# Optimization experiments

Hardware: AMD Instinct MI355X
Metric: run time of the kernel (lower is better)

The kernel has to match this reference:

```python
import jax, jax.numpy as jnp
import numpy as np

N, C, P, M = 8, 20, 8732, 16
THRESHOLD, NEG_POS_RATIO, ALPHA = 0.5, 3, 1.0


def cxcy_to_xy(c):
    return jnp.concatenate([c[..., :2] - c[..., 2:] / 2.0, c[..., :2] + c[..., 2:] / 2.0], axis=-1)


def xy_to_cxcy(xy):
    return jnp.concatenate([(xy[..., :2] + xy[..., 2:]) / 2.0, xy[..., 2:] - xy[..., :2]], axis=-1)


def cxcy_to_gcxgcy(cxcy, priors):
    g_cxcy = (cxcy[..., :2] - priors[..., :2]) / (priors[..., 2:] / 10.0)
    g_wh = jnp.log(cxcy[..., 2:] / priors[..., 2:]) * 5.0
    return jnp.concatenate([g_cxcy, g_wh], axis=-1)


def jaccard(a, b):
    # a: (M,4), b: (P,4), boundary coords -> IoU (M,P)
    lo = jnp.maximum(a[:, None, :2], b[None, :, :2])
    hi = jnp.minimum(a[:, None, 2:], b[None, :, 2:])
    inter = jnp.prod(jnp.clip(hi - lo, 0.0), axis=-1)
    area_a = jnp.prod(a[:, 2:] - a[:, :2], axis=-1)
    area_b = jnp.prod(b[:, 2:] - b[:, :2], axis=-1)
    return inter / (area_a[:, None] + area_b[None, :] - inter)


def setup_inputs() -> dict:
    key = jax.random.key(0)
    k1, k2, k3, k4, k5, k6 = jax.random.split(key, 6)
    predicted_locs = jax.random.normal(k1, (N, C, P, 4), jnp.float32)
    predicted_scores = jax.random.normal(k2, (N, C, P, 2), jnp.float32)
    # valid ground-truth boundary boxes (x1<x2, y1<y2) in [0,1]
    ctr = jax.random.uniform(k3, (N, C, M, 2), minval=0.2, maxval=0.8)
    wh = jax.random.uniform(k4, (N, C, M, 2), minval=0.05, maxval=0.3)
    boxes = jnp.concatenate([ctr - wh / 2.0, ctr + wh / 2.0], axis=-1)
    # valid priors in cxcywh (w,h > 0 so log-encoding is finite)
    pctr = jax.random.uniform(k5, (P, 2), minval=0.05, maxval=0.95)
    pwh = jax.random.uniform(k6, (P, 2), minval=0.05, maxval=0.5)
    priors_cxcy = jnp.concatenate([pctr, pwh], axis=-1)
    labels = jnp.ones((N, C, M), jnp.int32)  # binary per-class head: object label = 1
    return {
        "predicted_locs": predicted_locs,
        "predicted_scores": predicted_scores,
        "boxes": boxes,
        "labels": labels,
        "priors_cxcy": priors_cxcy,
    }


def _forward(predicted_locs, predicted_scores, boxes, priors_cxcy, labels):
    n_classes = predicted_scores.shape[1]
    n_priors = predicted_scores.shape[2]
    priors_xy = cxcy_to_xy(priors_cxcy)

    def match(b, lab):
        # b: (M,4) boundary, lab: (M,) int
        ov = jaccard(b, priors_xy)                       # (M,P)
        obj_for_prior = jnp.argmax(ov, axis=0)           # (P,)
        ov_for_prior = jnp.max(ov, axis=0)               # (P,)
        prior_for_obj = jnp.argmax(ov, axis=1)           # (M,)
        # force each object to own its best prior
        obj_for_prior = obj_for_prior.at[prior_for_obj].set(jnp.arange(b.shape[0]))
        ov_for_prior = ov_for_prior.at[prior_for_obj].set(1.0)
        cls = jnp.where(ov_for_prior < THRESHOLD, 0, lab[obj_for_prior])  # (P,)
        tl = cxcy_to_gcxgcy(xy_to_cxcy(b[obj_for_prior]), priors_cxcy)    # (P,4)
        return tl, cls

    true_locs, true_classes = jax.vmap(jax.vmap(match))(boxes, labels)  # (N,C,P,4), (N,C,P)

    pos = true_classes != 0                      # (N,C,P)
    posf = pos.astype(predicted_locs.dtype)
    n_pos_bc = posf.sum(axis=2)                  # (N,C) positives per image per class
    n_pos_c = n_pos_bc.sum(axis=0)               # (C,)

    # localization: mean L1 over positive priors (4 coords each), per class
    l1 = jnp.abs(predicted_locs - true_locs).sum(-1) * posf   # (N,C,P)
    loc_loss_c = l1.sum(axis=(0, 2)) / jnp.maximum(n_pos_c * 4.0, 1.0)

    # per-prior binary cross entropy
    logp = jax.nn.log_softmax(predicted_scores, axis=-1)      # (N,C,P,2)
    ce = -jnp.take_along_axis(logp, true_classes[..., None], axis=-1)[..., 0]  # (N,C,P)
    conf_pos_c = (ce * posf).sum(axis=(0, 2))

    # hard negative mining: sort negatives desc per (image,class) row, keep top 3*n_pos
    ce_neg = jnp.where(pos, 0.0, ce)
    ce_neg_sorted = -jnp.sort(-ce_neg, axis=-1)               # (N,C,P) descending
    n_hard = NEG_POS_RATIO * n_pos_bc                         # (N,C)
    ranks = jnp.arange(n_priors, dtype=n_hard.dtype)
    hard_mask = ranks[None, None, :] < n_hard[..., None]
    conf_hard_c = (ce_neg_sorted * hard_mask).sum(axis=(0, 2))

    safe = jnp.maximum(n_pos_c, 1.0)
    loss_c = jnp.where(
        n_pos_c > 0,
        (conf_pos_c + conf_hard_c + ALPHA * loc_loss_c) / safe,
        0.0,
    ) / n_classes
    return loss_c.sum()


def reference(predicted_locs, predicted_scores, boxes, labels, priors_cxcy):
    return _forward(predicted_locs, predicted_scores, boxes, priors_cxcy, labels)
```

## Files before the change

kernel.cpp:

```cpp
#include <hip/hip_runtime.h>
#include <math.h>

#define NN 8
#define CC 20
#define PP 8732
#define MM 16
#define NPR 3
#define ROWS (NN * CC)
#define SPLIT 12
#define CH 728
#define ABLK 256
#define FBLK 1024
#define EPT 9

#define OFF_PART  5588480
#define OFF_CST   5834240
#define OFF_RST   5857280
#define OFF_CNT   5862400

__device__ __forceinline__ float fast_rcp(float x) { return __builtin_amdgcn_rcpf(x); }
__device__ __forceinline__ float rfl(float x) {
    return __uint_as_float(__builtin_amdgcn_readfirstlane(__float_as_uint(x)));
}

__device__ __forceinline__ float lse2(float a, float b) {
    float mx = fmaxf(a, b);
    float d  = fabsf(a - b);
    return mx + __logf(1.0f + __expf(-d));
}

__global__ __launch_bounds__(ABLK) void mbox_p1(
    const float* __restrict__ locs, const float* __restrict__ scores,
    const float* __restrict__ boxes, const int* __restrict__ labels,
    const float* __restrict__ priors,
    float* __restrict__ cef,
    unsigned long long* __restrict__ partials, float* __restrict__ cstats,
    int* __restrict__ donecnt)
{
    const int row = blockIdx.x / SPLIT;
    const int chunk = blockIdx.x - row * SPLIT;
    const int tid = threadIdx.x, lane = tid & 63, wav = tid >> 6;

    if (blockIdx.x == 0 && tid == 0) *donecnt = 0;

    __shared__ float s_bcx[MM], s_bcy[MM], s_bw[MM], s_bh[MM];
    __shared__ unsigned int s_pk[4 * MM];
    __shared__ float s_rf[4 * 3];

    float bx1[MM], by1[MM], bx2[MM], by2[MM], bar[MM];
    unsigned int labm = 0;
    {
        const float* bb = boxes + (size_t)row * MM * 4;
        const int*   lb = labels + (size_t)row * MM;
#pragma unroll
        for (int m = 0; m < MM; m++) {
            float x1 = rfl(bb[m * 4 + 0]), y1 = rfl(bb[m * 4 + 1]);
            float x2 = rfl(bb[m * 4 + 2]), y2 = rfl(bb[m * 4 + 3]);
            bx1[m] = x1; by1[m] = y1; bx2[m] = x2; by2[m] = y2;
            bar[m] = rfl((x2 - x1) * (y2 - y1));
            labm |= (lb[m] != 0 ? 1u : 0u) << m;
        }
        labm = __builtin_amdgcn_readfirstlane(labm);
    }
    if (tid < MM) {
        s_bcx[tid] = (bx1[tid] + bx2[tid]) * 0.5f;
        s_bcy[tid] = (by1[tid] + by2[tid]) * 0.5f;
        s_bw[tid]  = bx2[tid] - bx1[tid];
        s_bh[tid]  = by2[tid] - by1[tid];
    }
    __syncthreads();

    const float4* pri4 = (const float4*)priors;
    const float4* loc4 = (const float4*)(locs + (size_t)row * PP * 4);
    const float2* sc2  = (const float2*)(scores + (size_t)row * PP * 2);
    float* cefr        = cef + (size_t)row * PP;

    unsigned int bestk[MM];
#pragma unroll
    for (int m = 0; m < MM; m++) bestk[m] = 0u;
    float l_np = 0.0f, l_l1 = 0.0f, l_cp = 0.0f;
    const int p0 = chunk * CH, p1e = min(p0 + CH, PP);

    float4 pr_next; float2 sc_next;
    if (p0 + tid < p1e) { pr_next = pri4[p0 + tid]; sc_next = sc2[p0 + tid]; }
    int it = 0;
    for (int p = p0 + tid; p < p1e; p += ABLK, ++it) {
        float4 pr = pr_next;
        float2 sc = sc_next;
        if (p + ABLK < p1e) { pr_next = pri4[p + ABLK]; sc_next = sc2[p + ABLK]; }
        const unsigned int lowb = ((unsigned int)(7 - it) << 8) | (unsigned int)(255 - tid);
        float hw = pr.z * 0.5f, hh = pr.w * 0.5f;
        float px1 = pr.x - hw, py1 = pr.y - hh;
        float px2 = pr.x + hw, py2 = pr.y + hh;
        float area_b = (px2 - px1) * (py2 - py1);
        unsigned int bovk = 0u;
#pragma unroll
        for (int m = 0; m < MM; m++) {
            float dx = fminf(bx2[m], px2) - fmaxf(bx1[m], px1);
            float dy = fminf(by2[m], py2) - fmaxf(by1[m], py1);
            dx = fmaxf(dx, 0.0f); dy = fmaxf(dy, 0.0f);
            float inter = dx * dy;
            float den = (bar[m] + area_b) - inter;
            float iou = inter * fast_rcp(den);
            unsigned int ib = __float_as_uint(iou);
            bovk = max(bovk, (ib & 0xFFFFFFF0u) | (unsigned int)(15 - m));
            bestk[m] = max(bestk[m], (ib & 0xFFFFF800u) | lowb);
        }
        int bm = 15 - (int)(bovk & 15u);
        bool pos = (bovk >= 0x3F000000u) && (((labm >> bm) & 1u) != 0u);
        float lse = lse2(sc.x, sc.y);
        float ce;
        if (pos) {
            float4 pl = loc4[p];
            l_np += 1.0f;
            l_cp += lse - sc.y;
            float tx = (s_bcx[bm] - pr.x) * 10.0f / pr.z;
            float ty = (s_bcy[bm] - pr.y) * 10.0f / pr.w;
            float tw = __logf(s_bw[bm] / pr.z) * 5.0f;
            float th = __logf(s_bh[bm] / pr.w) * 5.0f;
            l_l1 += fabsf(pl.x - tx) + fabsf(pl.y - ty) + fabsf(pl.z - tw) + fabsf(pl.w - th);
            ce = 0.0f;
        } else {
            ce = fmaxf(lse - sc.x, 0.0f);
        }
        cefr[p] = ce;
    }

#pragma unroll
    for (int m = 0; m < MM; m++) {
        unsigned int key = bestk[m];
#pragma unroll
        for (int off = 32; off; off >>= 1) {
            unsigned int o = __shfl_down(key, off);
            if (o > key) key = o;
        }
        if (lane == 0) s_pk[wav * MM + m] = key;
    }
#pragma unroll
    for (int off = 32; off; off >>= 1) {
        l_np += __shfl_down(l_np, off);
        l_l1 += __shfl_down(l_l1, off);
        l_cp += __shfl_down(l_cp, off);
    }
    if (lane == 0) { s_rf[wav * 3] = l_np; s_rf[wav * 3 + 1] = l_l1; s_rf[wav * 3 + 2] = l_cp; }
    __syncthreads();
    if (tid < MM) {
        unsigned int key = s_pk[tid];
        for (int w = 1; w < 4; w++) {
            unsigned int o = s_pk[w * MM + tid];
            if (o > key) key = o;
        }
        int tw  = 255 - (int)(key & 255u);
        int itw = 7 - (int)((key >> 8) & 7u);
        int pm  = p0 + itw * ABLK + tw;
        partials[((size_t)row * MM + tid) * SPLIT + chunk] =
            ((unsigned long long)(key & 0xFFFFF800u) << 32) |
            (unsigned int)(0x7fffffff - pm);
    }
    if (tid == 0) {
        float np = 0, l1 = 0, cp = 0;
        for (int w = 0; w < 4; w++) { np += s_rf[w * 3]; l1 += s_rf[w * 3 + 1]; cp += s_rf[w * 3 + 2]; }
        float* cs = cstats + ((size_t)row * SPLIT + chunk) * 3;
        cs[0] = np; cs[1] = l1; cs[2] = cp;
    }
}

__global__ __launch_bounds__(FBLK) void mbox_sel(
    const float* __restrict__ locs, const float* __restrict__ scores,
    const float* __restrict__ boxes, const int* __restrict__ labels,
    const float* __restrict__ priors,
    const float* __restrict__ cef,
    const unsigned long long* __restrict__ partials,
    const float* __restrict__ cstats, float* __restrict__ rstats,
    int* __restrict__ donecnt, float* __restrict__ out)
{
    const int row = blockIdx.x, tid = threadIdx.x, lane = tid & 63, wav = tid >> 6;

    __shared__ unsigned int s_u32[PP];
    __shared__ float s_bx1[MM], s_by1[MM], s_bx2[MM], s_by2[MM], s_bar[MM];
    __shared__ float s_bcx[MM], s_bcy[MM], s_bw[MM], s_bh[MM];
    __shared__ int s_lab[MM], s_pfo[MM];
    __shared__ float s_sum[3];
    __shared__ unsigned int s_hist[256];
    __shared__ unsigned int s_prefix, s_Kr, s_K;
    __shared__ float s_redf[16];
    __shared__ int s_redi[16];
    __shared__ int s_flag;

    if (tid < MM) {
        const float* b = boxes + ((size_t)row * MM + tid) * 4;
        float x1 = b[0], y1 = b[1], x2 = b[2], y2 = b[3];
        s_bx1[tid] = x1; s_by1[tid] = y1; s_bx2[tid] = x2; s_by2[tid] = y2;
        s_bar[tid] = (x2 - x1) * (y2 - y1);
        s_bcx[tid] = (x1 + x2) * 0.5f; s_bcy[tid] = (y1 + y2) * 0.5f;
        s_bw[tid] = x2 - x1; s_bh[tid] = y2 - y1;
        s_lab[tid] = labels[row * MM + tid];
        const unsigned long long* pr = partials + ((size_t)row * MM + tid) * SPLIT;
        unsigned long long key = pr[0];
        for (int c = 1; c < SPLIT; c++) { unsigned long long o = pr[c]; if (o > key) key = o; }
        s_pfo[tid] = 0x7fffffff - (int)(unsigned)(key & 0xffffffffull);
    }
    if (tid >= 16 && tid < 19) {
        int j = tid - 16; float s = 0;
        for (int c = 0; c < SPLIT; c++) s += cstats[((size_t)row * SPLIT + c) * 3 + j];
        s_sum[j] = s;
    }
#pragma unroll
    for (int k = 0; k < EPT; k++) {
        const int p = tid + k * FBLK;
        if (p < PP) s_u32[p] = __float_as_uint(cef[(size_t)row * PP + p]);
    }
    __syncthreads();

    const float4* pri4 = (const float4*)priors;
    const float4* loc4 = (const float4*)(locs + (size_t)row * PP * 4);
    const float2* sc2  = (const float2*)(scores + (size_t)row * PP * 2);
    float d_np = 0, d_l1 = 0, d_cp = 0;
    if (tid < MM) {
        int p = s_pfo[tid];
        bool is_last = true;
        for (int mm = tid + 1; mm < MM; mm++) if (s_pfo[mm] == p) is_last = false;
        if (is_last) {
            const float4 pr = pri4[p];
            const float4 pl = loc4[p];
            const float2 sc = sc2[p];
            float lse = lse2(sc.x, sc.y);
            float hw = pr.z * 0.5f, hh = pr.w * 0.5f;
            float px1 = pr.x - hw, py1 = pr.y - hh;
            float px2 = pr.x + hw, py2 = pr.y + hh;
            float area_b = (px2 - px1) * (py2 - py1);
            unsigned int bovk = 0u;
            for (int m = 0; m < MM; m++) {
                float dx = fminf(s_bx2[m], px2) - fmaxf(s_bx1[m], px1);
                float dy = fminf(s_by2[m], py2) - fmaxf(s_by1[m], py1);
                dx = fmaxf(dx, 0.0f); dy = fmaxf(dy, 0.0f);
                float inter = dx * dy;
                float den = (s_bar[m] + area_b) - inter;
                float iou = inter * fast_rcp(den);
                unsigned int ib = __float_as_uint(iou);
                bovk = max(bovk, (ib & 0xFFFFFFF0u) | (unsigned int)(15 - m));
            }
            int mo = 15 - (int)(bovk & 15u);
            bool waspos = (bovk >= 0x3F000000u) && (s_lab[mo] != 0);
            if (waspos) {
                d_np -= 1.0f; d_cp -= (lse - sc.y);
                float tx = (s_bcx[mo] - pr.x) * 10.0f / pr.z;
                float ty = (s_bcy[mo] - pr.y) * 10.0f / pr.w;
                float tw = __logf(s_bw[mo] / pr.z) * 5.0f;
                float th = __logf(s_bh[mo] / pr.w) * 5.0f;
                d_l1 -= fabsf(pl.x - tx) + fabsf(pl.y - ty) + fabsf(pl.z - tw) + fabsf(pl.w - th);
            }
            if (s_lab[tid] != 0) {
                d_np += 1.0f; d_cp += (lse - sc.y);
                float tx = (s_bcx[tid] - pr.x) * 10.0f / pr.z;
                float ty = (s_bcy[tid] - pr.y) * 10.0f / pr.w;
                float tw = __logf(s_bw[tid] / pr.z) * 5.0f;
                float th = __logf(s_bh[tid] / pr.w) * 5.0f;
                d_l1 += fabsf(pl.x - tx) + fabsf(pl.y - ty) + fabsf(pl.z - tw) + fabsf(pl.w - th);
                s_u32[p] = 0u;
            } else {
                s_u32[p] = __float_as_uint(fmaxf(lse - sc.x, 0.0f));
            }
        }
    }
    if (tid < 64) {
#pragma unroll
        for (int off = 32; off; off >>= 1) {
            d_np += __shfl_down(d_np, off);
            d_l1 += __shfl_down(d_l1, off);
            d_cp += __shfl_down(d_cp, off);
        }
        if (tid == 0) {
            float np = s_sum[0] + d_np;
            __hip_atomic_store(&rstats[(size_t)row * 8 + 0], np,
                               __ATOMIC_RELAXED, __HIP_MEMORY_SCOPE_AGENT);
            __hip_atomic_store(&rstats[(size_t)row * 8 + 1], s_sum[1] + d_l1,
                               __ATOMIC_RELAXED, __HIP_MEMORY_SCOPE_AGENT);
            __hip_atomic_store(&rstats[(size_t)row * 8 + 2], s_sum[2] + d_cp,
                               __ATOMIC_RELAXED, __HIP_MEMORY_SCOPE_AGENT);
            int K = NPR * (int)(np + 0.5f);
            s_K = (K > 0) ? (unsigned)K : 0u;
            s_prefix = 0u;
            s_Kr = (K > 0) ? (unsigned)K : 0u;
        }
    }
    __syncthreads();

    const unsigned int K = s_K;
    unsigned int T = 0u;
    if (K > 0u && K < PP) {
        for (int pass = 0; pass < 4; pass++) {
            const int shift = 24 - 8 * pass;
            if (tid < 256) s_hist[tid] = 0u;
            __syncthreads();
            const unsigned int pref   = s_prefix;
            const unsigned int maskhi = (pass == 0) ? 0u : (0xffffffffu << (shift + 8));
#pragma unroll
            for (int k = 0; k < EPT; k++) {
                const int p = tid + k * FBLK;
                unsigned int u = (p < PP) ? s_u32[p] : 0u;
                if ((u & maskhi) == pref) atomicAdd(&s_hist[(u >> shift) & 255u], 1u);
            }
            __syncthreads();
            if (wav == 0) {
                unsigned int Kr = s_Kr;
                unsigned int h0 = s_hist[lane * 4 + 0];
                unsigned int h1 = s_hist[lane * 4 + 1];
                unsigned int h2 = s_hist[lane * 4 + 2];
                unsigned int h3 = s_hist[lane * 4 + 3];
                unsigned int c3 = h3;
                unsigned int c2 = h3 + h2;
                unsigned int c1 = c2 + h1;
                unsigned int c0 = c1 + h0;
                unsigned int suf = c0;
#pragma unroll
                for (int off = 1; off < 64; off <<= 1) {
                    unsigned int o = __shfl_down(suf, off);
                    if (lane + off < 64) suf += o;
                }
                unsigned int above = suf - c0;
                int cand = -1;
                unsigned int G = 0;
                if      (c3 + above >= Kr) { cand = lane * 4 + 3; G = above + c3 - h3; }
                else if (c2 + above >= Kr) { cand = lane * 4 + 2; G = above + c2 - h2; }
                else if (c1 + above >= Kr) { cand = lane * 4 + 1; G = above + c1 - h1; }
                else if (c0 + above >= Kr) { cand = lane * 4 + 0; G = above + c0 - h0; }
                int best = cand;
#pragma unroll
                for (int off = 32; off; off >>= 1) best = max(best, __shfl_down(best, off));
                best = __shfl(best, 0);
                if (cand == best && cand >= 0) {
                    s_Kr = Kr - G;
                    s_prefix = pref | ((unsigned int)best << shift);
                }
            }
            __syncthreads();
        }
        T = s_prefix;
    }

    float sgt = 0.0f; int cgt = 0;
    if (K > 0u) {
#pragma unroll
        for (int k = 0; k < EPT; k++) {
            const int p = tid + k * FBLK;
            unsigned int u = (p < PP) ? s_u32[p] : 0u;
            if (u > T) { sgt += __uint_as_float(u); cgt++; }
        }
    }
#pragma unroll
    for (int off = 32; off; off >>= 1) {
        sgt += __shfl_down(sgt, off);
        cgt += __shfl_down(cgt, off);
    }
    if (lane == 0) { s_redf[wav] = sgt; s_redi[wav] = cgt; }
    __syncthreads();
    if (tid == 0) {
        float s = 0; int cnt = 0;
        for (int w = 0; w < 16; w++) { s += s_redf[w]; cnt += s_redi[w]; }
        float chard = (K > 0u) ? (s + (float)(int)(K - (unsigned)cnt) * __uint_as_float(T)) : 0.0f;
        __hip_atomic_store(&rstats[(size_t)row * 8 + 4], chard,
                           __ATOMIC_RELAXED, __HIP_MEMORY_SCOPE_AGENT);
        int old = __hip_atomic_fetch_add(donecnt, 1, __ATOMIC_ACQ_REL,
                                         __HIP_MEMORY_SCOPE_AGENT);
        s_flag = (old == ROWS - 1) ? 1 : 0;
    }
    __syncthreads();
    if (!s_flag) return;

    if (tid < 64) {
        int c = tid;
        float loss = 0.0f;
        if (c < CC) {
            float np = 0, l1 = 0, cp = 0, ch = 0;
            for (int n = 0; n < NN; n++) {
                const float* s = rstats + ((size_t)(n * CC + c)) * 8;
                np += __hip_atomic_load(&s[0], __ATOMIC_ACQUIRE, __HIP_MEMORY_SCOPE_AGENT);
                l1 += __hip_atomic_load(&s[1], __ATOMIC_ACQUIRE, __HIP_MEMORY_SCOPE_AGENT);
                cp += __hip_atomic_load(&s[2], __ATOMIC_ACQUIRE, __HIP_MEMORY_SCOPE_AGENT);
                ch += __hip_atomic_load(&s[4], __ATOMIC_ACQUIRE, __HIP_MEMORY_SCOPE_AGENT);
            }
            float loc = l1 / fmaxf(np * 4.0f, 1.0f);
            float val = (np > 0.0f) ? (cp + ch + loc) / fmaxf(np, 1.0f) : 0.0f;
            loss = val / (float)CC;
        }
#pragma unroll
        for (int off = 32; off; off >>= 1) loss += __shfl_down(loss, off);
        if (tid == 0) out[0] = loss;
    }
}

extern "C" void kernel_launch(void* const* d_in, const int* in_sizes, int n_in,
                              void* d_out, int out_size, void* d_ws, size_t ws_size,
                              hipStream_t stream) {
    const float* locs   = (const float*)d_in[0];
    const float* scores = (const float*)d_in[1];
    const float* boxes  = (const float*)d_in[2];
    const int*   labels = (const int*)d_in[3];
    const float* priors = (const float*)d_in[4];
    float* out = (float*)d_out;

    char* ws = (char*)d_ws;
    float* cef                   = (float*)ws;
    unsigned long long* partials = (unsigned long long*)(ws + OFF_PART);
    float* cstats                = (float*)(ws + OFF_CST);
    float* rstats                = (float*)(ws + OFF_RST);
    int* donecnt                 = (int*)(ws + OFF_CNT);

    mbox_p1<<<ROWS * SPLIT, ABLK, 0, stream>>>(locs, scores, boxes, labels, priors,
                                               cef, partials, cstats, donecnt);
    mbox_sel<<<ROWS, FBLK, 0, stream>>>(locs, scores, boxes, labels, priors,
                                        cef, partials, cstats, rstats, donecnt, out);
}
```

Baseline: 128.7 us.

## Halve p1 split, vectorize cef load, per-wave histograms, separate finalize kernel

Reduces the matching kernel split from 12 to 6 chunks per row, so each block covers twice as many priors. The selection kernel now loads its scores into LDS with uint4 vector loads. The radix-select histogram becomes 16 per-wave copies to cut LDS atomic contention, at the cost of an extra merge step and sync per pass. The last-block done-counter with atomics is replaced by a third tiny finalize kernel, which adds a launch but removes the global atomic and fence traffic.

```diff
diff --git a/kernel.cpp b/kernel.cpp
--- a/kernel.cpp
+++ b/kernel.cpp
@@ -7,16 +7,16 @@
 #define MM 16
 #define NPR 3
 #define ROWS (NN * CC)
-#define SPLIT 12
-#define CH 728
+#define SPLIT 6
+#define CH 1456
 #define ABLK 256
 #define FBLK 1024
 #define EPT 9
+#define NV4 2183
 
 #define OFF_PART  5588480
-#define OFF_CST   5834240
-#define OFF_RST   5857280
-#define OFF_CNT   5862400
+#define OFF_CST   5711360
+#define OFF_RST   5722880
 
 __device__ __forceinline__ float fast_rcp(float x) { return __builtin_amdgcn_rcpf(x); }
 __device__ __forceinline__ float rfl(float x) {
@@ -34,14 +34,11 @@
     const float* __restrict__ boxes, const int* __restrict__ labels,
     const float* __restrict__ priors,
     float* __restrict__ cef,
-    unsigned long long* __restrict__ partials, float* __restrict__ cstats,
-    int* __restrict__ donecnt)
+    unsigned long long* __restrict__ partials, float* __restrict__ cstats)
 {
     const int row = blockIdx.x / SPLIT;
     const int chunk = blockIdx.x - row * SPLIT;
     const int tid = threadIdx.x, lane = tid & 63, wav = tid >> 6;
-
-    if (blockIdx.x == 0 && tid == 0) *donecnt = 0;
 
     __shared__ float s_bcx[MM], s_bcy[MM], s_bw[MM], s_bh[MM];
     __shared__ unsigned int s_pk[4 * MM];
@@ -171,21 +168,20 @@
     const float* __restrict__ priors,
     const float* __restrict__ cef,
     const unsigned long long* __restrict__ partials,
-    const float* __restrict__ cstats, float* __restrict__ rstats,
-    int* __restrict__ donecnt, float* __restrict__ out)
+    const float* __restrict__ cstats, float* __restrict__ rstats)
 {
     const int row = blockIdx.x, tid = threadIdx.x, lane = tid & 63, wav = tid >> 6;
 
     __shared__ unsigned int s_u32[PP];
+    __shared__ unsigned int s_hist[16][257];
+    __shared__ unsigned int s_h[256];
     __shared__ float s_bx1[MM], s_by1[MM], s_bx2[MM], s_by2[MM], s_bar[MM];
     __shared__ float s_bcx[MM], s_bcy[MM], s_bw[MM], s_bh[MM];
     __shared__ int s_lab[MM], s_pfo[MM];
     __shared__ float s_sum[3];
-    __shared__ unsigned int s_hist[256];
     __shared__ unsigned int s_prefix, s_Kr, s_K;
     __shared__ float s_redf[16];
     __shared__ int s_redi[16];
-    __shared__ int s_flag;
 
     if (tid < MM) {
         const float* b = boxes + ((size_t)row * MM + tid) * 4;
@@ -205,10 +201,14 @@
         for (int c = 0; c < SPLIT; c++) s += cstats[((size_t)row * SPLIT + c) * 3 + j];
         s_sum[j] = s;
     }
-#pragma unroll
-    for (int k = 0; k < EPT; k++) {
-        const int p = tid + k * FBLK;
-        if (p < PP) s_u32[p] = __float_as_uint(cef[(size_t)row * PP + p]);
+    {
+        const uint4* c4 = (const uint4*)(cef + (size_t)row * PP);
+        uint4* l4 = (uint4*)s_u32;
+#pragma unroll
+        for (int k = 0; k < 3; k++) {
+            const int i = tid + k * FBLK;
+            if (i < NV4) l4[i] = c4[i];
+        }
     }
     __syncthreads();
 
@@ -272,12 +272,9 @@
         }
         if (tid == 0) {
             float np = s_sum[0] + d_np;
-            __hip_atomic_store(&rstats[(size_t)row * 8 + 0], np,
-                               __ATOMIC_RELAXED, __HIP_MEMORY_SCOPE_AGENT);
-            __hip_atomic_store(&rstats[(size_t)row * 8 + 1], s_sum[1] + d_l1,
-                               __ATOMIC_RELAXED, __HIP_MEMORY_SCOPE_AGENT);
-            __hip_atomic_store(&rstats[(size_t)row * 8 + 2], s_sum[2] + d_cp,
-                               __ATOMIC_RELAXED, __HIP_MEMORY_SCOPE_AGENT);
+            rstats[(size_t)row * 8 + 0] = np;
+            rstats[(size_t)row * 8 + 1] = s_sum[1] + d_l1;
+            rstats[(size_t)row * 8 + 2] = s_sum[2] + d_cp;
             int K = NPR * (int)(np + 0.5f);
             s_K = (K > 0) ? (unsigned)K : 0u;
             s_prefix = 0u;
@@ -291,7 +288,7 @@
     if (K > 0u && K < PP) {
         for (int pass = 0; pass < 4; pass++) {
             const int shift = 24 - 8 * pass;
-            if (tid < 256) s_hist[tid] = 0u;
+            for (int i = tid; i < 16 * 257; i += FBLK) ((unsigned int*)s_hist)[i] = 0u;
             __syncthreads();
             const unsigned int pref   = s_prefix;
             const unsigned int maskhi = (pass == 0) ? 0u : (0xffffffffu << (shift + 8));
@@ -299,15 +296,22 @@
             for (int k = 0; k < EPT; k++) {
                 const int p = tid + k * FBLK;
                 unsigned int u = (p < PP) ? s_u32[p] : 0u;
-                if ((u & maskhi) == pref) atomicAdd(&s_hist[(u >> shift) & 255u], 1u);
+                if ((u & maskhi) == pref) atomicAdd(&s_hist[wav][(u >> shift) & 255u], 1u);
+            }
+            __syncthreads();
+            if (tid < 256) {
+                unsigned int t = 0;
+#pragma unroll
+                for (int w = 0; w < 16; w++) t += s_hist[w][tid];
+                s_h[tid] = t;
             }
             __syncthreads();
             if (wav == 0) {
                 unsigned int Kr = s_Kr;
-                unsigned int h0 = s_hist[lane * 4 + 0];
-                unsigned int h1 = s_hist[lane * 4 + 1];
-                unsigned int h2 = s_hist[lane * 4 + 2];
-                unsigned int h3 = s_hist[lane * 4 + 3];
+                unsigned int h0 = s_h[lane * 4 + 0];
+                unsigned int h1 = s_h[lane * 4 + 1];
+                unsigned int h2 = s_h[lane * 4 + 2];
+                unsigned int h3 = s_h[lane * 4 + 3];
                 unsigned int c3 = h3;
                 unsigned int c2 = h3 + h2;
                 unsigned int c1 = c2 + h1;
@@ -359,35 +363,26 @@
         float s = 0; int cnt = 0;
         for (int w = 0; w < 16; w++) { s += s_redf[w]; cnt += s_redi[w]; }
         float chard = (K > 0u) ? (s + (float)(int)(K - (unsigned)cnt) * __uint_as_float(T)) : 0.0f;
-        __hip_atomic_store(&rstats[(size_t)row * 8 + 4], chard,
-                           __ATOMIC_RELAXED, __HIP_MEMORY_SCOPE_AGENT);
-        int old = __hip_atomic_fetch_add(donecnt, 1, __ATOMIC_ACQ_REL,
-                                         __HIP_MEMORY_SCOPE_AGENT);
-        s_flag = (old == ROWS - 1) ? 1 : 0;
-    }
-    __syncthreads();
-    if (!s_flag) return;
-
-    if (tid < 64) {
-        int c = tid;
-        float loss = 0.0f;
-        if (c < CC) {
-            float np = 0, l1 = 0, cp = 0, ch = 0;
-            for (int n = 0; n < NN; n++) {
-                const float* s = rstats + ((size_t)(n * CC + c)) * 8;
-                np += __hip_atomic_load(&s[0], __ATOMIC_ACQUIRE, __HIP_MEMORY_SCOPE_AGENT);
-                l1 += __hip_atomic_load(&s[1], __ATOMIC_ACQUIRE, __HIP_MEMORY_SCOPE_AGENT);
-                cp += __hip_atomic_load(&s[2], __ATOMIC_ACQUIRE, __HIP_MEMORY_SCOPE_AGENT);
-                ch += __hip_atomic_load(&s[4], __ATOMIC_ACQUIRE, __HIP_MEMORY_SCOPE_AGENT);
-            }
-            float loc = l1 / fmaxf(np * 4.0f, 1.0f);
-            float val = (np > 0.0f) ? (cp + ch + loc) / fmaxf(np, 1.0f) : 0.0f;
-            loss = val / (float)CC;
-        }
-#pragma unroll
-        for (int off = 32; off; off >>= 1) loss += __shfl_down(loss, off);
-        if (tid == 0) out[0] = loss;
-    }
+        rstats[(size_t)row * 8 + 4] = chard;
+    }
+}
+
+__global__ void mbox_finalize(const float* __restrict__ rstats, float* __restrict__ out) {
+    int c = threadIdx.x;
+    float loss = 0.0f;
+    if (c < CC) {
+        float np = 0, l1 = 0, cp = 0, ch = 0;
+        for (int n = 0; n < NN; n++) {
+            const float* s = rstats + ((size_t)(n * CC + c)) * 8;
+            np += s[0]; l1 += s[1]; cp += s[2]; ch += s[4];
+        }
+        float loc = l1 / fmaxf(np * 4.0f, 1.0f);
+        float val = (np > 0.0f) ? (cp + ch + loc) / fmaxf(np, 1.0f) : 0.0f;
+        loss = val / (float)CC;
+    }
+#pragma unroll
+    for (int off = 32; off; off >>= 1) loss += __shfl_down(loss, off);
+    if (threadIdx.x == 0) out[0] = loss;
 }
 
 extern "C" void kernel_launch(void* const* d_in, const int* in_sizes, int n_in,
@@ -405,10 +400,10 @@
     unsigned long long* partials = (unsigned long long*)(ws + OFF_PART);
     float* cstats                = (float*)(ws + OFF_CST);
     float* rstats                = (float*)(ws + OFF_RST);
-    int* donecnt                 = (int*)(ws + OFF_CNT);
 
     mbox_p1<<<ROWS * SPLIT, ABLK, 0, stream>>>(locs, scores, boxes, labels, priors,
-                                               cef, partials, cstats, donecnt);
+                                               cef, partials, cstats);
     mbox_sel<<<ROWS, FBLK, 0, stream>>>(locs, scores, boxes, labels, priors,
-                                        cef, partials, cstats, rstats, donecnt, out);
-}
+                                        cef, partials, cstats, rstats);
+    mbox_finalize<<<1, 64, 0, stream>>>(rstats, out);
+}
```

New measurement: 120.2 us (median of 2 runs). 1.07x faster.
